# Kernel tuning notes

Measured on AMD Instinct MI355X. Metric: run time of the kernel, lower is better.

## Reference

```python
import jax, jax.numpy as jnp
import numpy as np

# Dimensions
B, T = 4, 512
STOCH = 1024          # flattened stochastic latent dim
D_MODEL = 512
N_LAYER = 4
N_ACT = 16            # discrete action vocab
D_STATE = 16          # SSM state size
K_CONV = 4            # depthwise causal conv width
EXPAND = 2
D_INNER = EXPAND * D_MODEL  # 1024
DT_RANK = D_MODEL // 16     # 32
EPS = 1e-5


def _layer_norm(x, w, b):
    m = jnp.mean(x, axis=-1, keepdims=True)
    v = jnp.mean(jnp.square(x - m), axis=-1, keepdims=True)
    return (x - m) * jax.lax.rsqrt(v + EPS) * w + b


def _mamba_block(x, W_in_l, conv_w_l, conv_b_l, W_xproj_l, W_dt_l, b_dt_l, A_log_l, D_l, W_out_l):
    """Mamba-1 selective-scan block. x: (B,T,d_model) -> (B,T,d_model)."""
    bsz = x.shape[0]
    xz = x @ W_in_l                      # (B,T,2*d_inner)
    xin, z = jnp.split(xz, 2, axis=-1)
    # causal depthwise conv over time
    xc = jnp.transpose(xin, (0, 2, 1))   # (B,d_inner,T)
    xc = jax.lax.conv_general_dilated(
        xc, conv_w_l[:, None, :], (1,), [(K_CONV - 1, 0)],
        dimension_numbers=("NCH", "OIH", "NCH"), feature_group_count=D_INNER)
    xc = xc + conv_b_l[None, :, None]
    xc = jax.nn.silu(jnp.transpose(xc, (0, 2, 1)))   # (B,T,d_inner)
    # input-dependent dt, B, C
    dbc = xc @ W_xproj_l                 # (B,T,dt_rank+2*d_state)
    dt_raw = dbc[..., :DT_RANK]
    Bm = dbc[..., DT_RANK:DT_RANK + D_STATE]
    Cm = dbc[..., DT_RANK + D_STATE:]
    dt = jax.nn.softplus(dt_raw @ W_dt_l + b_dt_l)   # (B,T,d_inner)
    A = -jnp.exp(A_log_l)                # (d_inner,d_state)

    def step(h, inp):
        x_t, dt_t, B_t, C_t = inp        # (B,di),(B,di),(B,ds),(B,ds)
        dA = jnp.exp(dt_t[..., None] * A)                       # (B,di,ds)
        h = dA * h + (dt_t * x_t)[..., None] * B_t[:, None, :]  # (B,di,ds)
        y = jnp.einsum("bds,bs->bd", h, C_t)
        return h, y

    h0 = jnp.zeros((bsz, D_INNER, D_STATE), x.dtype)
    xs = (jnp.swapaxes(xc, 0, 1), jnp.swapaxes(dt, 0, 1),
          jnp.swapaxes(Bm, 0, 1), jnp.swapaxes(Cm, 0, 1))
    _, ys = jax.lax.scan(step, h0, xs)                  # (T,B,d_inner)
    y = jnp.swapaxes(ys, 0, 1) + D_l * xc               # skip connection
    y = y * jax.nn.silu(z)                              # gate
    return y @ W_out_l


def setup_inputs() -> dict:
    key = jax.random.key(0)
    ks = jax.random.split(key, 12)

    def nrm(k, shape, s=0.02):
        return jax.random.normal(k, shape, dtype=jnp.float32) * s

    return {
        "samples": jax.random.normal(ks[0], (B, T, STOCH), dtype=jnp.float32),
        "actions": jax.random.randint(ks[1], (B, T), 0, N_ACT),
        "W_embed": nrm(ks[2], (STOCH, D_MODEL)),
        "b_embed": jnp.zeros((D_MODEL,), jnp.float32),
        "act_embed": nrm(ks[3], (N_ACT, D_MODEL)),
        "ln_w": jnp.ones((N_LAYER, D_MODEL), jnp.float32),
        "ln_b": jnp.zeros((N_LAYER, D_MODEL), jnp.float32),
        "W_in": nrm(ks[4], (N_LAYER, D_MODEL, 2 * D_INNER)),
        "conv_w": nrm(ks[5], (N_LAYER, D_INNER, K_CONV), 0.1),
        "conv_b": jnp.zeros((N_LAYER, D_INNER), jnp.float32),
        "W_xproj": nrm(ks[6], (N_LAYER, D_INNER, DT_RANK + 2 * D_STATE)),
        "W_dt": nrm(ks[7], (N_LAYER, DT_RANK, D_INNER), 0.1),
        "b_dt": jnp.full((N_LAYER, D_INNER), -4.6, jnp.float32),  # softplus ~ 0.01
        "A_log": jnp.log(jnp.broadcast_to(
            jnp.arange(1, D_STATE + 1, dtype=jnp.float32), (N_LAYER, D_INNER, D_STATE))),
        "D_skip": jnp.ones((N_LAYER, D_INNER), jnp.float32),
        "W_out": nrm(ks[8], (N_LAYER, D_INNER, D_MODEL)),
        "normf_w": jnp.ones((D_MODEL,), jnp.float32),
        "normf_b": jnp.zeros((D_MODEL,), jnp.float32),
        "out_ln_w": jnp.ones((D_MODEL,), jnp.float32),
        "out_ln_b": jnp.zeros((D_MODEL,), jnp.float32),
    }


def reference(samples, actions, W_embed, b_embed, act_embed, ln_w, ln_b, W_in,
              conv_w, conv_b, W_xproj, W_dt, b_dt, A_log, D_skip, W_out,
              normf_w, normf_b, out_ln_w, out_ln_b):
    # embed stochastic latent + action token
    x = samples @ W_embed + b_embed + act_embed[actions]   # (B,T,d_model)
    for l in range(N_LAYER):  # structurally distinct layer params; small fixed loop
        x = x + _mamba_block(_layer_norm(x, ln_w[l], ln_b[l]),
                             W_in[l], conv_w[l], conv_b[l], W_xproj[l],
                             W_dt[l], b_dt[l], A_log[l], D_skip[l], W_out[l])
    x = _layer_norm(x, normf_w, normf_b)     # backbone final norm
    x = _layer_norm(x, out_ln_w, out_ln_b)   # adapter output_norm
    return jnp.mean(x, axis=1)               # mean pool over time -> (B,d_model)
```

## Files before the change

### kernel.cpp

```cpp
#include <hip/hip_runtime.h>
#include <hip/hip_bf16.h>
#include <math.h>

#define B_    4
#define T_    512
#define BT    2048
#define STOCH 1024
#define DM    512
#define DI    1024
#define DS    16
#define DTR   32
#define KC    4
#define NL    4
#define EPSV  1e-5f
#define CH    32
#define TC    16
#define SK2   16
#define GKS   4

typedef short bf16x8 __attribute__((ext_vector_type(8)));
typedef float f32x4  __attribute__((ext_vector_type(4)));

__device__ __forceinline__ ushort bfbits(float f) {
    uint u = __float_as_uint(f);
    u += 0x7FFFu + ((u >> 16) & 1u);
    return (ushort)(u >> 16);
}

__global__ __launch_bounds__(256)
void wconvT(const float* __restrict__ W, short* __restrict__ Wt, int K, int N)
{
    const float* Wb = W + (size_t)blockIdx.z * K * N;
    short* Wtb = Wt + (size_t)blockIdx.z * K * N;
    __shared__ float tile[32][33];
    const int tx = threadIdx.x, ty = threadIdx.y;
    const int n0 = blockIdx.x * 32, k0 = blockIdx.y * 32;
    #pragma unroll
    for (int j = 0; j < 4; j++)
        tile[ty + j * 8][tx] = Wb[(size_t)(k0 + ty + j * 8) * N + n0 + tx];
    __syncthreads();
    #pragma unroll
    for (int j = 0; j < 4; j++) {
        const int n = ty + j * 8;
        Wtb[(size_t)(n0 + n) * K + k0 + tx] = (short)bfbits(tile[tx][n]);
    }
}

__global__ __launch_bounds__(256, 4)
void gemm_mfma_sk(const float* __restrict__ A, int lda,
                  const short* __restrict__ Wt, int ldw,
                  float* __restrict__ part, int Ncols, size_t strideZ,
                  int Ksl)
{
    constexpr int BM = 64, BN = 64;
    __shared__ short As[2][BM][40];
    __shared__ short Bs[2][BN][40];
    const int tid = threadIdx.x;
    const int wave = tid >> 6, lane = tid & 63;
    const int lr = lane & 15, lg = lane >> 4;
    const int wm0 = (wave >> 1) * 32, wn0 = (wave & 1) * 32;
    const int bm = blockIdx.y * BM, bn = blockIdx.x * BN;
    const int kbase = blockIdx.z * Ksl;

    f32x4 acc[2][2];
    #pragma unroll
    for (int fi = 0; fi < 2; fi++)
        #pragma unroll
        for (int fj = 0; fj < 2; fj++)
            acc[fi][fj] = (f32x4){0.f, 0.f, 0.f, 0.f};

    float4 ar0, ar1; uint4 br0;
    const int arow0 = tid >> 3, aseg0 = tid & 7;
    const int brow  = tid >> 2, bseg  = tid & 3;

    auto loadT = [&](int k0) {
        ar0 = *reinterpret_cast<const float4*>(A + (size_t)(bm + arow0) * lda + k0 + aseg0 * 4);
        ar1 = *reinterpret_cast<const float4*>(A + (size_t)(bm + arow0 + 32) * lda + k0 + aseg0 * 4);
        br0 = *reinterpret_cast<const uint4*>(Wt + (size_t)(bn + brow) * ldw + k0 + bseg * 8);
    };
    auto storeT = [&](int buf) {
        uint2 p;
        p.x = (uint)bfbits(ar0.x) | ((uint)bfbits(ar0.y) << 16);
        p.y = (uint)bfbits(ar0.z) | ((uint)bfbits(ar0.w) << 16);
        *reinterpret_cast<uint2*>(&As[buf][arow0][aseg0 * 4]) = p;
        p.x = (uint)bfbits(ar1.x) | ((uint)bfbits(ar1.y) << 16);
        p.y = (uint)bfbits(ar1.z) | ((uint)bfbits(ar1.w) << 16);
        *reinterpret_cast<uint2*>(&As[buf][arow0 + 32][aseg0 * 4]) = p;
        *reinterpret_cast<uint4*>(&Bs[buf][brow][bseg * 8]) = br0;
    };

    loadT(kbase);
    storeT(0);
    const int NK = Ksl >> 5;
    for (int kk = 0; kk < NK; kk++) {
        const int cur = kk & 1;
        if (kk + 1 < NK) loadT(kbase + (kk + 1) * 32);
        __syncthreads();
        bf16x8 af[2], bfr[2];
        #pragma unroll
        for (int fi = 0; fi < 2; fi++)
            af[fi] = *reinterpret_cast<const bf16x8*>(&As[cur][wm0 + fi * 16 + lr][lg * 8]);
        #pragma unroll
        for (int fj = 0; fj < 2; fj++)
            bfr[fj] = *reinterpret_cast<const bf16x8*>(&Bs[cur][wn0 + fj * 16 + lr][lg * 8]);
        #pragma unroll
        for (int fi = 0; fi < 2; fi++)
            #pragma unroll
            for (int fj = 0; fj < 2; fj++)
                acc[fi][fj] = __builtin_amdgcn_mfma_f32_16x16x32_bf16(
                    af[fi], bfr[fj], acc[fi][fj], 0, 0, 0);
        if (kk + 1 < NK) storeT(cur ^ 1);
    }

    float* P = part + (size_t)blockIdx.z * strideZ;
    #pragma unroll
    for (int fi = 0; fi < 2; fi++)
        #pragma unroll
        for (int fj = 0; fj < 2; fj++)
            #pragma unroll
            for (int r = 0; r < 4; r++) {
                const int m = bm + wm0 + fi * 16 + lg * 4 + r;
                const int n = bn + wn0 + fj * 16 + lr;
                P[(size_t)m * Ncols + n] = acc[fi][fj][r];
            }
}

__global__ __launch_bounds__(256, 4)
void gemm_mfma_db(const float* __restrict__ A, int lda,
                  const short* __restrict__ Wt, int ldw,
                  float* __restrict__ C, int ldc, int Kd)
{
    constexpr int BM = 64, BN = 64;
    __shared__ short As[2][BM][40];
    __shared__ short Bs[2][BN][40];
    const int tid = threadIdx.x;
    const int wave = tid >> 6, lane = tid & 63;
    const int lr = lane & 15, lg = lane >> 4;
    const int wm0 = (wave >> 1) * 32, wn0 = (wave & 1) * 32;
    const int bm = blockIdx.y * BM, bn = blockIdx.x * BN;

    f32x4 acc[2][2];
    #pragma unroll
    for (int fi = 0; fi < 2; fi++)
        #pragma unroll
        for (int fj = 0; fj < 2; fj++)
            acc[fi][fj] = (f32x4){0.f, 0.f, 0.f, 0.f};

    float4 ar0, ar1; uint4 br0;
    const int arow0 = tid >> 3, aseg0 = tid & 7;
    const int brow  = tid >> 2, bseg  = tid & 3;

    auto loadT = [&](int k0) {
        ar0 = *reinterpret_cast<const float4*>(A + (size_t)(bm + arow0) * lda + k0 + aseg0 * 4);
        ar1 = *reinterpret_cast<const float4*>(A + (size_t)(bm + arow0 + 32) * lda + k0 + aseg0 * 4);
        br0 = *reinterpret_cast<const uint4*>(Wt + (size_t)(bn + brow) * ldw + k0 + bseg * 8);
    };
    auto storeT = [&](int buf) {
        uint2 p;
        p.x = (uint)bfbits(ar0.x) | ((uint)bfbits(ar0.y) << 16);
        p.y = (uint)bfbits(ar0.z) | ((uint)bfbits(ar0.w) << 16);
        *reinterpret_cast<uint2*>(&As[buf][arow0][aseg0 * 4]) = p;
        p.x = (uint)bfbits(ar1.x) | ((uint)bfbits(ar1.y) << 16);
        p.y = (uint)bfbits(ar1.z) | ((uint)bfbits(ar1.w) << 16);
        *reinterpret_cast<uint2*>(&As[buf][arow0 + 32][aseg0 * 4]) = p;
        *reinterpret_cast<uint4*>(&Bs[buf][brow][bseg * 8]) = br0;
    };

    loadT(0);
    storeT(0);
    const int NK = Kd >> 5;
    for (int kk = 0; kk < NK; kk++) {
        const int cur = kk & 1;
        if (kk + 1 < NK) loadT((kk + 1) * 32);
        __syncthreads();
        bf16x8 af[2], bfr[2];
        #pragma unroll
        for (int fi = 0; fi < 2; fi++)
            af[fi] = *reinterpret_cast<const bf16x8*>(&As[cur][wm0 + fi * 16 + lr][lg * 8]);
        #pragma unroll
        for (int fj = 0; fj < 2; fj++)
            bfr[fj] = *reinterpret_cast<const bf16x8*>(&Bs[cur][wn0 + fj * 16 + lr][lg * 8]);
        #pragma unroll
        for (int fi = 0; fi < 2; fi++)
            #pragma unroll
            for (int fj = 0; fj < 2; fj++)
                acc[fi][fj] = __builtin_amdgcn_mfma_f32_16x16x32_bf16(
                    af[fi], bfr[fj], acc[fi][fj], 0, 0, 0);
        if (kk + 1 < NK) storeT(cur ^ 1);
    }

    #pragma unroll
    for (int fi = 0; fi < 2; fi++)
        #pragma unroll
        for (int fj = 0; fj < 2; fj++)
            #pragma unroll
            for (int r = 0; r < 4; r++) {
                const int m = bm + wm0 + fi * 16 + lg * 4 + r;
                const int n = bn + wn0 + fj * 16 + lr;
                C[(size_t)m * ldc + n] = acc[fi][fj][r];
            }
}

__global__ __launch_bounds__(256, 2)
void xprojconv(const float* __restrict__ xz, const float* __restrict__ cw,
               const float* __restrict__ cb, const short* __restrict__ WxT,
               float* __restrict__ xc, float* __restrict__ part)
{
    __shared__ short As[64][40];
    __shared__ short Bs[64][40];
    const int tid = threadIdx.x;
    const int sk = blockIdx.x;
    const int bm = blockIdx.y * 64;
    const int wave = tid >> 6, lane = tid & 63;
    const int lr = lane & 15, lg = lane >> 4;
    const int wm0 = (wave >> 1) * 32, wn0 = (wave & 1) * 32;

    f32x4 acc[2][2];
    #pragma unroll
    for (int fi = 0; fi < 2; fi++)
        #pragma unroll
        for (int fj = 0; fj < 2; fj++)
            acc[fi][fj] = (f32x4){0.f, 0.f, 0.f, 0.f};

    for (int kk = 0; kk < 2; kk++) {
        #pragma unroll
        for (int g = 0; g < 2; g++) {
            const int gi = tid + g * 256;
            const int row = gi >> 3, seg = gi & 7;
            const int bt = bm + row, t = bt & (T_ - 1);
            const int d4 = sk * 64 + kk * 32 + seg * 4;
            const float4 z = {0.f, 0.f, 0.f, 0.f};
            const float4 L0 = *reinterpret_cast<const float4*>(xz + (size_t)bt * 2048 + d4);
            const float4 L1 = (t >= 1) ? *reinterpret_cast<const float4*>(xz + (size_t)(bt - 1) * 2048 + d4) : z;
            const float4 L2 = (t >= 2) ? *reinterpret_cast<const float4*>(xz + (size_t)(bt - 2) * 2048 + d4) : z;
            const float4 L3 = (t >= 3) ? *reinterpret_cast<const float4*>(xz + (size_t)(bt - 3) * 2048 + d4) : z;
            const float4 cbv = *reinterpret_cast<const float4*>(cb + d4);
            float4 o;
            {
                const float4 w = *reinterpret_cast<const float4*>(cw + (size_t)(d4 + 0) * 4);
                o.x = cbv.x + w.w * L0.x + w.z * L1.x + w.y * L2.x + w.x * L3.x;
            }
            {
                const float4 w = *reinterpret_cast<const float4*>(cw + (size_t)(d4 + 1) * 4);
                o.y = cbv.y + w.w * L0.y + w.z * L1.y + w.y * L2.y + w.x * L3.y;
            }
            {
                const float4 w = *reinterpret_cast<const float4*>(cw + (size_t)(d4 + 2) * 4);
                o.z = cbv.z + w.w * L0.z + w.z * L1.z + w.y * L2.z + w.x * L3.z;
            }
            {
                const float4 w = *reinterpret_cast<const float4*>(cw + (size_t)(d4 + 3) * 4);
                o.w = cbv.w + w.w * L0.w + w.z * L1.w + w.y * L2.w + w.x * L3.w;
            }
            o.x *= 1.f / (1.f + __expf(-o.x));
            o.y *= 1.f / (1.f + __expf(-o.y));
            o.z *= 1.f / (1.f + __expf(-o.z));
            o.w *= 1.f / (1.f + __expf(-o.w));
            *reinterpret_cast<float4*>(xc + (size_t)bt * DI + d4) = o;
            uint2 p;
            p.x = (uint)bfbits(o.x) | ((uint)bfbits(o.y) << 16);
            p.y = (uint)bfbits(o.z) | ((uint)bfbits(o.w) << 16);
            *reinterpret_cast<uint2*>(&As[row][seg * 4]) = p;
        }
        {
            const int row = tid >> 2, seg = tid & 3;
            *reinterpret_cast<uint4*>(&Bs[row][seg * 8]) =
                *reinterpret_cast<const uint4*>(WxT + (size_t)row * DI + sk * 64 + kk * 32 + seg * 8);
        }
        __syncthreads();
        bf16x8 af[2], bfr[2];
        #pragma unroll
        for (int fi = 0; fi < 2; fi++)
            af[fi] = *reinterpret_cast<const bf16x8*>(&As[wm0 + fi * 16 + lr][lg * 8]);
        #pragma unroll
        for (int fj = 0; fj < 2; fj++)
            bfr[fj] = *reinterpret_cast<const bf16x8*>(&Bs[wn0 + fj * 16 + lr][lg * 8]);
        #pragma unroll
        for (int fi = 0; fi < 2; fi++)
            #pragma unroll
            for (int fj = 0; fj < 2; fj++)
                acc[fi][fj] = __builtin_amdgcn_mfma_f32_16x16x32_bf16(
                    af[fi], bfr[fj], acc[fi][fj], 0, 0, 0);
        __syncthreads();
    }

    float* P = part + (size_t)sk * (BT * 64);
    #pragma unroll
    for (int fi = 0; fi < 2; fi++)
        #pragma unroll
        for (int fj = 0; fj < 2; fj++)
            #pragma unroll
            for (int r = 0; r < 4; r++) {
                const int m = bm + wm0 + fi * 16 + lg * 4 + r;
                const int n = wn0 + fj * 16 + lr;
                P[(size_t)m * 64 + n] = acc[fi][fj][r];
            }
}

__global__ __launch_bounds__(256)
void dtred(const float* __restrict__ part, const short* __restrict__ WdT,
           const float* __restrict__ b_dt, float* __restrict__ dbc,
           float* __restrict__ dtb)
{
    __shared__ short As[64][40];
    __shared__ short Bs[64][40];
    const int tid = threadIdx.x;
    const int nb = blockIdx.x;
    const int m0 = blockIdx.y * 64, n0 = nb * 64;
    const int wave = tid >> 6, lane = tid & 63;
    const int lr = lane & 15, lg = lane >> 4;
    const int wm0 = (wave >> 1) * 32, wn0 = (wave & 1) * 32;

    #pragma unroll
    for (int g = 0; g < 2; g++) {
        const int gi = tid + g * 256;
        const int row = gi >> 3, seg = gi & 7;
        float4 s = {0.f, 0.f, 0.f, 0.f};
        #pragma unroll
        for (int z = 0; z < SK2; z++) {
            const float4 p = *reinterpret_cast<const float4*>(
                part + (size_t)z * (BT * 64) + (size_t)(m0 + row) * 64 + seg * 4);
            s.x += p.x; s.y += p.y; s.z += p.z; s.w += p.w;
        }
        uint2 pk;
        pk.x = (uint)bfbits(s.x) | ((uint)bfbits(s.y) << 16);
        pk.y = (uint)bfbits(s.z) | ((uint)bfbits(s.w) << 16);
        *reinterpret_cast<uint2*>(&As[row][seg * 4]) = pk;
    }
    {
        const int row = tid >> 2, seg = tid & 3;
        *reinterpret_cast<uint4*>(&Bs[row][seg * 8]) =
            *reinterpret_cast<const uint4*>(WdT + (size_t)(n0 + row) * DTR + seg * 8);
    }
    if (nb == 0) {
        #pragma unroll
        for (int g = 0; g < 2; g++) {
            const int gi = tid + g * 256;
            const int row = gi >> 3, seg = gi & 7;
            float4 s = {0.f, 0.f, 0.f, 0.f};
            #pragma unroll
            for (int z = 0; z < SK2; z++) {
                const float4 p = *reinterpret_cast<const float4*>(
                    part + (size_t)z * (BT * 64) + (size_t)(m0 + row) * 64 + 32 + seg * 4);
                s.x += p.x; s.y += p.y; s.z += p.z; s.w += p.w;
            }
            *reinterpret_cast<float4*>(dbc + (size_t)(m0 + row) * 64 + 32 + seg * 4) = s;
        }
    }
    __syncthreads();

    bf16x8 af[2], bfr[2];
    f32x4 acc[2][2];
    #pragma unroll
    for (int fi = 0; fi < 2; fi++)
        #pragma unroll
        for (int fj = 0; fj < 2; fj++)
            acc[fi][fj] = (f32x4){0.f, 0.f, 0.f, 0.f};
    #pragma unroll
    for (int fi = 0; fi < 2; fi++)
        af[fi] = *reinterpret_cast<const bf16x8*>(&As[wm0 + fi * 16 + lr][lg * 8]);
    #pragma unroll
    for (int fj = 0; fj < 2; fj++)
        bfr[fj] = *reinterpret_cast<const bf16x8*>(&Bs[wn0 + fj * 16 + lr][lg * 8]);
    #pragma unroll
    for (int fi = 0; fi < 2; fi++)
        #pragma unroll
        for (int fj = 0; fj < 2; fj++)
            acc[fi][fj] = __builtin_amdgcn_mfma_f32_16x16x32_bf16(
                af[fi], bfr[fj], acc[fi][fj], 0, 0, 0);
    #pragma unroll
    for (int fi = 0; fi < 2; fi++)
        #pragma unroll
        for (int fj = 0; fj < 2; fj++)
            #pragma unroll
            for (int r = 0; r < 4; r++) {
                const int m = m0 + wm0 + fi * 16 + lg * 4 + r;
                const int n = n0 + wn0 + fj * 16 + lr;
                float v = acc[fi][fj][r] + b_dt[n];
                v = fmaxf(v, 0.f) + log1pf(__expf(-fabsf(v)));
                dtb[(size_t)m * DI + n] = v;
            }
}

__global__ __launch_bounds__(256)
void scan_passA(const float* __restrict__ dt, const float* __restrict__ xc,
                const float* __restrict__ dbc, const float* __restrict__ A_log,
                float* __restrict__ Aprod, float* __restrict__ hloc)
{
    const int blk = blockIdx.x;
    const int dg = blk & 3;
    const int c  = (blk >> 2) & (CH - 1);
    const int b  = blk >> 7;
    const int d  = dg * 256 + threadIdx.x;
    const size_t base = (size_t)b * T_ + c * TC;

    __shared__ float Bsh[TC][DS];
    {
        const int t = threadIdx.x >> 4, s = threadIdx.x & 15;
        Bsh[t][s] = dbc[(base + t) * 64 + 32 + s];
    }
    __syncthreads();

    float Aval[DS], h[DS], ap[DS];
    #pragma unroll
    for (int s = 0; s < DS; s++) {
        Aval[s] = -__expf(A_log[(size_t)d * DS + s]);
        h[s] = 0.f; ap[s] = 1.f;
    }

    #pragma unroll 4
    for (int t = 0; t < TC; t++) {
        const size_t r = base + t;
        const float dtv = dt[r * DI + d];
        const float xv  = xc[r * DI + d];
        const float u = dtv * xv;
        #pragma unroll
        for (int s = 0; s < DS; s++) {
            const float a = __expf(dtv * Aval[s]);
            h[s] = a * h[s] + u * Bsh[t][s];
            ap[s] *= a;
        }
    }
    const size_t o0 = ((size_t)(b * CH + c) * DS) * DI + d;
    #pragma unroll
    for (int s = 0; s < DS; s++) {
        Aprod[o0 + (size_t)s * DI] = ap[s];
        hloc[o0 + (size_t)s * DI]  = h[s];
    }
}

__global__ __launch_bounds__(256)
void scan_passB(const float* __restrict__ Aprod, float* __restrict__ hloc)
{
    const int idx = blockIdx.x * 256 + threadIdx.x;
    const int d = idx & (DI - 1);
    const int s = (idx >> 10) & (DS - 1);
    const int b = idx >> 14;
    float h = 0.f;
    for (int c = 0; c < CH; c++) {
        const size_t o = ((size_t)(b * CH + c) * DS + s) * DI + d;
        const float a  = Aprod[o];
        const float hl = hloc[o];
        hloc[o] = h;
        h = a * h + hl;
    }
}

__global__ __launch_bounds__(256)
void scan_passC(const float* __restrict__ dt, const float* __restrict__ xc,
                const float* __restrict__ dbc, const float* __restrict__ xz,
                const float* __restrict__ A_log, const float* __restrict__ Dskip,
                const float* __restrict__ h0buf, float* __restrict__ y)
{
    const int blk = blockIdx.x;
    const int dg = blk & 3;
    const int c  = (blk >> 2) & (CH - 1);
    const int b  = blk >> 7;
    const int d  = dg * 256 + threadIdx.x;
    const size_t base = (size_t)b * T_ + c * TC;

    __shared__ float Bsh[TC][DS];
    __shared__ float Csh[TC][DS];
    for (int i = threadIdx.x; i < TC * 32; i += 256) {
        const int t = i >> 5, sc = i & 31;
        const float v = dbc[(base + t) * 64 + 32 + sc];
        if (sc < 16) Bsh[t][sc] = v; else Csh[t][sc - 16] = v;
    }
    __syncthreads();

    float Aval[DS], h[DS];
    const size_t o0 = ((size_t)(b * CH + c) * DS) * DI + d;
    #pragma unroll
    for (int s = 0; s < DS; s++) {
        Aval[s] = -__expf(A_log[(size_t)d * DS + s]);
        h[s] = h0buf[o0 + (size_t)s * DI];
    }
    const float Dv = Dskip[d];

    #pragma unroll 2
    for (int t = 0; t < TC; t++) {
        const size_t r = base + t;
        const float dtv = dt[r * DI + d];
        const float xv  = xc[r * DI + d];
        const float u = dtv * xv;
        float yacc = 0.f;
        #pragma unroll
        for (int s = 0; s < DS; s++) {
            const float a = __expf(dtv * Aval[s]);
            h[s] = a * h[s] + u * Bsh[t][s];
            yacc += h[s] * Csh[t][s];
        }
        const float zv = xz[r * 2048 + 1024 + d];
        const float sg = 1.f / (1.f + __expf(-zv));
        y[r * DI + d] = (yacc + Dv * xv) * (zv * sg);
    }
}

template<int MODE>
__global__ __launch_bounds__(256)
void red_ln(const float* __restrict__ part, float* __restrict__ x,
            float* __restrict__ hout,
            const float* __restrict__ e1, const float* __restrict__ e2,
            const int* __restrict__ act,
            const float* __restrict__ w1, const float* __restrict__ b1,
            const float* __restrict__ w2, const float* __restrict__ b2)
{
    const int row = blockIdx.x, tid = threadIdx.x;
    const size_t ro = (size_t)row * DM;
    __shared__ float sm[4], sm2[4];
    float v[2];
    float s = 0.f, ss = 0.f;
    #pragma unroll
    for (int g = 0; g < 2; g++) {
        const int c = tid + g * 256;
        float t = 0.f;
        #pragma unroll
        for (int z = 0; z < GKS; z++) t += part[(size_t)z * (BT * DM) + ro + c];
        if (MODE == 0) t += e1[c] + e2[(size_t)act[row] * DM + c];
        else           t += x[ro + c];
        if (MODE != 2) x[ro + c] = t;
        v[g] = t; s += t; ss += t * t;
    }
    #pragma unroll
    for (int m = 32; m >= 1; m >>= 1) { s += __shfl_xor(s, m, 64); ss += __shfl_xor(ss, m, 64); }
    if ((tid & 63) == 0) { sm[tid >> 6] = s; sm2[tid >> 6] = ss; }
    __syncthreads();
    s  = sm[0] + sm[1] + sm[2] + sm[3];
    ss = sm2[0] + sm2[1] + sm2[2] + sm2[3];
    float mean = s * (1.f / DM);
    float var = fmaxf(ss * (1.f / DM) - mean * mean, 0.f);
    float rstd = rsqrtf(var + EPSV);
    if (MODE < 2) {
        #pragma unroll
        for (int g = 0; g < 2; g++) {
            const int c = tid + g * 256;
            hout[ro + c] = (v[g] - mean) * rstd * w1[c] + b1[c];
        }
    } else {
        float u[2]; float s2 = 0.f, ss2 = 0.f;
        #pragma unroll
        for (int g = 0; g < 2; g++) {
            const int c = tid + g * 256;
            u[g] = (v[g] - mean) * rstd * w1[c] + b1[c];
            s2 += u[g]; ss2 += u[g] * u[g];
        }
        #pragma unroll
        for (int m = 32; m >= 1; m >>= 1) { s2 += __shfl_xor(s2, m, 64); ss2 += __shfl_xor(ss2, m, 64); }
        __syncthreads();
        if ((tid & 63) == 0) { sm[tid >> 6] = s2; sm2[tid >> 6] = ss2; }
        __syncthreads();
        s2  = sm[0] + sm[1] + sm[2] + sm[3];
        ss2 = sm2[0] + sm2[1] + sm2[2] + sm2[3];
        float mean2 = s2 * (1.f / DM);
        float var2 = fmaxf(ss2 * (1.f / DM) - mean2 * mean2, 0.f);
        float rstd2 = rsqrtf(var2 + EPSV);
        #pragma unroll
        for (int g = 0; g < 2; g++) {
            const int c = tid + g * 256;
            hout[ro + c] = (u[g] - mean2) * rstd2 * w2[c] + b2[c];
        }
    }
}

__global__ __launch_bounds__(256)
void mean_kernel(const float* __restrict__ x, float* __restrict__ out)
{
    const int idx = blockIdx.x * 256 + threadIdx.x;
    const int b = idx / DM;
    const int dcol = idx % DM;
    float ssum = 0.f;
    for (int t = 0; t < T_; t++) ssum += x[((size_t)b * T_ + t) * DM + dcol];
    out[idx] = ssum * (1.f / T_);
}

extern "C" void kernel_launch(void* const* d_in, const int* in_sizes, int n_in,
                              void* d_out, int out_size, void* d_ws, size_t ws_size,
                              hipStream_t stream)
{
    const float* samples  = (const float*)d_in[0];
    const int*   actions  = (const int*)  d_in[1];
    const float* W_embed  = (const float*)d_in[2];
    const float* b_embed  = (const float*)d_in[3];
    const float* act_emb  = (const float*)d_in[4];
    const float* ln_w     = (const float*)d_in[5];
    const float* ln_b     = (const float*)d_in[6];
    const float* W_in     = (const float*)d_in[7];
    const float* conv_w   = (const float*)d_in[8];
    const float* conv_b   = (const float*)d_in[9];
    const float* W_xproj  = (const float*)d_in[10];
    const float* W_dt     = (const float*)d_in[11];
    const float* b_dt     = (const float*)d_in[12];
    const float* A_log    = (const float*)d_in[13];
    const float* D_skip   = (const float*)d_in[14];
    const float* W_out    = (const float*)d_in[15];
    const float* normf_w  = (const float*)d_in[16];
    const float* normf_b  = (const float*)d_in[17];
    const float* out_ln_w = (const float*)d_in[18];
    const float* out_ln_b = (const float*)d_in[19];

    float* ws  = (float*)d_ws;
    float* x    = ws;
    float* h    = x    + (size_t)BT * DM;
    float* xz   = h    + (size_t)BT * DM;
    float* xc   = xz   + (size_t)BT * 2048;
    float* dbc  = xc   + (size_t)BT * DI;
    float* dtb  = dbc  + (size_t)BT * 64;
    float* yg   = dtb  + (size_t)BT * DI;
    float* Apr  = yg   + (size_t)BT * DI;
    float* hlo  = Apr  + (size_t)B_ * CH * DI * DS;
    float* xpart = Apr;
    float* gpart = Apr;
    float* wb   = hlo  + (size_t)B_ * CH * DI * DS;
    short* WtE  = (short*)wb;
    short* WtI  = WtE + (size_t)DM * STOCH;
    short* WtO  = WtI + (size_t)4 * 2048 * DM;
    short* WxT  = WtO + (size_t)4 * DM * DI;
    short* WdT  = WxT + (size_t)4 * 64 * DI;

    const int MN = BT * DM;

    wconvT<<<dim3(DM / 32, STOCH / 32, 1), dim3(32, 8), 0, stream>>>(W_embed, WtE, STOCH, DM);
    wconvT<<<dim3(2048 / 32, DM / 32, 4), dim3(32, 8), 0, stream>>>(W_in, WtI, DM, 2048);
    wconvT<<<dim3(DM / 32, DI / 32, 4), dim3(32, 8), 0, stream>>>(W_out, WtO, DI, DM);
    wconvT<<<dim3(64 / 32, DI / 32, 4), dim3(32, 8), 0, stream>>>(W_xproj, WxT, DI, 64);
    wconvT<<<dim3(DI / 32, 1, 4), dim3(32, 8), 0, stream>>>(W_dt, WdT, DTR, DI);

    gemm_mfma_sk<<<dim3(DM / 64, BT / 64, GKS), 256, 0, stream>>>(
        samples, STOCH, WtE, STOCH, gpart, DM, (size_t)MN, STOCH / GKS);
    red_ln<0><<<BT, 256, 0, stream>>>(gpart, x, h, b_embed, act_emb, actions,
                                      ln_w, ln_b, nullptr, nullptr);

    for (int l = 0; l < NL; l++) {
        gemm_mfma_db<<<dim3(2048 / 64, BT / 64), 256, 0, stream>>>(
            h, DM, WtI + (size_t)l * 2048 * DM, DM, xz, 2048, DM);
        xprojconv<<<dim3(SK2, BT / 64), 256, 0, stream>>>(
            xz, conv_w + (size_t)l * DI * KC, conv_b + (size_t)l * DI,
            WxT + (size_t)l * 64 * DI, xc, xpart);
        dtred<<<dim3(16, BT / 64), 256, 0, stream>>>(
            xpart, WdT + (size_t)l * DI * DTR, b_dt + (size_t)l * DI, dbc, dtb);
        scan_passA<<<B_ * CH * (DI / 256), 256, 0, stream>>>(
            dtb, xc, dbc, A_log + (size_t)l * DI * DS, Apr, hlo);
        scan_passB<<<(B_ * DS * DI) / 256, 256, 0, stream>>>(Apr, hlo);
        scan_passC<<<B_ * CH * (DI / 256), 256, 0, stream>>>(
            dtb, xc, dbc, xz, A_log + (size_t)l * DI * DS, D_skip + (size_t)l * DI,
            hlo, yg);
        gemm_mfma_sk<<<dim3(DM / 64, BT / 64, GKS), 256, 0, stream>>>(
            yg, DI, WtO + (size_t)l * DM * DI, DI, gpart, DM, (size_t)MN, DI / GKS);
        if (l < NL - 1)
            red_ln<1><<<BT, 256, 0, stream>>>(gpart, x, h, nullptr, nullptr, nullptr,
                                              ln_w + (size_t)(l + 1) * DM,
                                              ln_b + (size_t)(l + 1) * DM,
                                              nullptr, nullptr);
        else
            red_ln<2><<<BT, 256, 0, stream>>>(gpart, x, yg, nullptr, nullptr, nullptr,
                                              normf_w, normf_b, out_ln_w, out_ln_b);
    }

    mean_kernel<<<(B_ * DM) / 256, 256, 0, stream>>>(yg, (float*)d_out);
}
```

Before: 467.0 us.

## Atomic-accumulate out-projection split-K into residual and merge weight conversion launches

The out-projection split-K GEMM now adds its partial sums straight into the residual stream x with float atomics, instead of writing four partial buffers that red_ln later reads and sums. red_ln in the layer modes then only reads x. Separately, the five weight transpose-and-convert launches are merged into one kernel that picks its source matrix from the block index. This removes partial-buffer traffic and launch overhead, but makes the summation order nondeterministic and adds atomic contention.

```diff
diff --git a/kernel.cpp b/kernel.cpp
--- a/kernel.cpp
+++ b/kernel.cpp
@@ -27,22 +27,42 @@
     return (ushort)(u >> 16);
 }
 
+#define TE_ 512
+#define TI_ 4096
+#define TO_ 2048
+#define TX_ 256
+#define TD_ 128
 __global__ __launch_bounds__(256)
-void wconvT(const float* __restrict__ W, short* __restrict__ Wt, int K, int N)
-{
-    const float* Wb = W + (size_t)blockIdx.z * K * N;
-    short* Wtb = Wt + (size_t)blockIdx.z * K * N;
+void wconvT_all(const float* __restrict__ We, short* __restrict__ WtE,
+                const float* __restrict__ Wi, short* __restrict__ WtI,
+                const float* __restrict__ Wo, short* __restrict__ WtO,
+                const float* __restrict__ Wx, short* __restrict__ WxT,
+                const float* __restrict__ Wd, short* __restrict__ WdT)
+{
+    int t = blockIdx.x;
+    const float* W; short* Wt; int K, N;
+    if (t < TE_)                         { W = We; Wt = WtE; K = STOCH; N = DM; }
+    else if ((t -= TE_) < TI_)           { W = Wi; Wt = WtI; K = DM;    N = 2048; }
+    else if ((t -= TI_) < TO_)           { W = Wo; Wt = WtO; K = DI;    N = DM; }
+    else if ((t -= TO_) < TX_)           { W = Wx; Wt = WxT; K = DI;    N = 64; }
+    else       { t -= TX_;                 W = Wd; Wt = WdT; K = DTR;   N = DI; }
+    const int ntx = N >> 5, per = (N >> 5) * (K >> 5);
+    const int batch = t / per;  t %= per;
+    const int bx = t % ntx, by = t / ntx;
+    W  += (size_t)batch * K * N;
+    Wt += (size_t)batch * K * N;
+
     __shared__ float tile[32][33];
     const int tx = threadIdx.x, ty = threadIdx.y;
-    const int n0 = blockIdx.x * 32, k0 = blockIdx.y * 32;
+    const int n0 = bx * 32, k0 = by * 32;
     #pragma unroll
     for (int j = 0; j < 4; j++)
-        tile[ty + j * 8][tx] = Wb[(size_t)(k0 + ty + j * 8) * N + n0 + tx];
+        tile[ty + j * 8][tx] = W[(size_t)(k0 + ty + j * 8) * N + n0 + tx];
     __syncthreads();
     #pragma unroll
     for (int j = 0; j < 4; j++) {
         const int n = ty + j * 8;
-        Wtb[(size_t)(n0 + n) * K + k0 + tx] = (short)bfbits(tile[tx][n]);
+        Wt[(size_t)(n0 + n) * K + k0 + tx] = (short)bfbits(tile[tx][n]);
     }
 }
 
@@ -126,9 +146,9 @@
 }
 
 __global__ __launch_bounds__(256, 4)
-void gemm_mfma_db(const float* __restrict__ A, int lda,
+void gemm_mfma_at(const float* __restrict__ A, int lda,
                   const short* __restrict__ Wt, int ldw,
-                  float* __restrict__ C, int ldc, int Kd)
+                  float* __restrict__ C, int Ncols, int Ksl)
 {
     constexpr int BM = 64, BN = 64;
     __shared__ short As[2][BM][40];
@@ -138,6 +158,7 @@
     const int lr = lane & 15, lg = lane >> 4;
     const int wm0 = (wave >> 1) * 32, wn0 = (wave & 1) * 32;
     const int bm = blockIdx.y * BM, bn = blockIdx.x * BN;
+    const int kbase = blockIdx.z * Ksl;
 
     f32x4 acc[2][2];
     #pragma unroll
@@ -166,6 +187,82 @@
         *reinterpret_cast<uint4*>(&Bs[buf][brow][bseg * 8]) = br0;
     };
 
+    loadT(kbase);
+    storeT(0);
+    const int NK = Ksl >> 5;
+    for (int kk = 0; kk < NK; kk++) {
+        const int cur = kk & 1;
+        if (kk + 1 < NK) loadT(kbase + (kk + 1) * 32);
+        __syncthreads();
+        bf16x8 af[2], bfr[2];
+        #pragma unroll
+        for (int fi = 0; fi < 2; fi++)
+            af[fi] = *reinterpret_cast<const bf16x8*>(&As[cur][wm0 + fi * 16 + lr][lg * 8]);
+        #pragma unroll
+        for (int fj = 0; fj < 2; fj++)
+            bfr[fj] = *reinterpret_cast<const bf16x8*>(&Bs[cur][wn0 + fj * 16 + lr][lg * 8]);
+        #pragma unroll
+        for (int fi = 0; fi < 2; fi++)
+            #pragma unroll
+            for (int fj = 0; fj < 2; fj++)
+                acc[fi][fj] = __builtin_amdgcn_mfma_f32_16x16x32_bf16(
+                    af[fi], bfr[fj], acc[fi][fj], 0, 0, 0);
+        if (kk + 1 < NK) storeT(cur ^ 1);
+    }
+
+    #pragma unroll
+    for (int fi = 0; fi < 2; fi++)
+        #pragma unroll
+        for (int fj = 0; fj < 2; fj++)
+            #pragma unroll
+            for (int r = 0; r < 4; r++) {
+                const int m = bm + wm0 + fi * 16 + lg * 4 + r;
+                const int n = bn + wn0 + fj * 16 + lr;
+                unsafeAtomicAdd(&C[(size_t)m * Ncols + n], acc[fi][fj][r]);
+            }
+}
+
+__global__ __launch_bounds__(256, 4)
+void gemm_mfma_db(const float* __restrict__ A, int lda,
+                  const short* __restrict__ Wt, int ldw,
+                  float* __restrict__ C, int ldc, int Kd)
+{
+    constexpr int BM = 64, BN = 64;
+    __shared__ short As[2][BM][40];
+    __shared__ short Bs[2][BN][40];
+    const int tid = threadIdx.x;
+    const int wave = tid >> 6, lane = tid & 63;
+    const int lr = lane & 15, lg = lane >> 4;
+    const int wm0 = (wave >> 1) * 32, wn0 = (wave & 1) * 32;
+    const int bm = blockIdx.y * BM, bn = blockIdx.x * BN;
+
+    f32x4 acc[2][2];
+    #pragma unroll
+    for (int fi = 0; fi < 2; fi++)
+        #pragma unroll
+        for (int fj = 0; fj < 2; fj++)
+            acc[fi][fj] = (f32x4){0.f, 0.f, 0.f, 0.f};
+
+    float4 ar0, ar1; uint4 br0;
+    const int arow0 = tid >> 3, aseg0 = tid & 7;
+    const int brow  = tid >> 2, bseg  = tid & 3;
+
+    auto loadT = [&](int k0) {
+        ar0 = *reinterpret_cast<const float4*>(A + (size_t)(bm + arow0) * lda + k0 + aseg0 * 4);
+        ar1 = *reinterpret_cast<const float4*>(A + (size_t)(bm + arow0 + 32) * lda + k0 + aseg0 * 4);
+        br0 = *reinterpret_cast<const uint4*>(Wt + (size_t)(bn + brow) * ldw + k0 + bseg * 8);
+    };
+    auto storeT = [&](int buf) {
+        uint2 p;
+        p.x = (uint)bfbits(ar0.x) | ((uint)bfbits(ar0.y) << 16);
+        p.y = (uint)bfbits(ar0.z) | ((uint)bfbits(ar0.w) << 16);
+        *reinterpret_cast<uint2*>(&As[buf][arow0][aseg0 * 4]) = p;
+        p.x = (uint)bfbits(ar1.x) | ((uint)bfbits(ar1.y) << 16);
+        p.y = (uint)bfbits(ar1.z) | ((uint)bfbits(ar1.w) << 16);
+        *reinterpret_cast<uint2*>(&As[buf][arow0 + 32][aseg0 * 4]) = p;
+        *reinterpret_cast<uint4*>(&Bs[buf][brow][bseg * 8]) = br0;
+    };
+
     loadT(0);
     storeT(0);
     const int NK = Kd >> 5;
@@ -513,12 +610,16 @@
     #pragma unroll
     for (int g = 0; g < 2; g++) {
         const int c = tid + g * 256;
-        float t = 0.f;
-        #pragma unroll
-        for (int z = 0; z < GKS; z++) t += part[(size_t)z * (BT * DM) + ro + c];
-        if (MODE == 0) t += e1[c] + e2[(size_t)act[row] * DM + c];
-        else           t += x[ro + c];
-        if (MODE != 2) x[ro + c] = t;
+        float t;
+        if (MODE == 0) {
+            t = 0.f;
+            #pragma unroll
+            for (int z = 0; z < GKS; z++) t += part[(size_t)z * (BT * DM) + ro + c];
+            t += e1[c] + e2[(size_t)act[row] * DM + c];
+            x[ro + c] = t;
+        } else {
+            t = x[ro + c];
+        }
         v[g] = t; s += t; ss += t * t;
     }
     #pragma unroll
@@ -619,11 +720,8 @@
 
     const int MN = BT * DM;
 
-    wconvT<<<dim3(DM / 32, STOCH / 32, 1), dim3(32, 8), 0, stream>>>(W_embed, WtE, STOCH, DM);
-    wconvT<<<dim3(2048 / 32, DM / 32, 4), dim3(32, 8), 0, stream>>>(W_in, WtI, DM, 2048);
-    wconvT<<<dim3(DM / 32, DI / 32, 4), dim3(32, 8), 0, stream>>>(W_out, WtO, DI, DM);
-    wconvT<<<dim3(64 / 32, DI / 32, 4), dim3(32, 8), 0, stream>>>(W_xproj, WxT, DI, 64);
-    wconvT<<<dim3(DI / 32, 1, 4), dim3(32, 8), 0, stream>>>(W_dt, WdT, DTR, DI);
+    wconvT_all<<<TE_ + TI_ + TO_ + TX_ + TD_, dim3(32, 8), 0, stream>>>(
+        W_embed, WtE, W_in, WtI, W_out, WtO, W_xproj, WxT, W_dt, WdT);
 
     gemm_mfma_sk<<<dim3(DM / 64, BT / 64, GKS), 256, 0, stream>>>(
         samples, STOCH, WtE, STOCH, gpart, DM, (size_t)MN, STOCH / GKS);
@@ -644,15 +742,15 @@
         scan_passC<<<B_ * CH * (DI / 256), 256, 0, stream>>>(
             dtb, xc, dbc, xz, A_log + (size_t)l * DI * DS, D_skip + (size_t)l * DI,
             hlo, yg);
-        gemm_mfma_sk<<<dim3(DM / 64, BT / 64, GKS), 256, 0, stream>>>(
-            yg, DI, WtO + (size_t)l * DM * DI, DI, gpart, DM, (size_t)MN, DI / GKS);
+        gemm_mfma_at<<<dim3(DM / 64, BT / 64, GKS), 256, 0, stream>>>(
+            yg, DI, WtO + (size_t)l * DM * DI, DI, x, DM, DI / GKS);
         if (l < NL - 1)
-            red_ln<1><<<BT, 256, 0, stream>>>(gpart, x, h, nullptr, nullptr, nullptr,
+            red_ln<1><<<BT, 256, 0, stream>>>(nullptr, x, h, nullptr, nullptr, nullptr,
                                               ln_w + (size_t)(l + 1) * DM,
                                               ln_b + (size_t)(l + 1) * DM,
                                               nullptr, nullptr);
         else
-            red_ln<2><<<BT, 256, 0, stream>>>(gpart, x, yg, nullptr, nullptr, nullptr,
+            red_ln<2><<<BT, 256, 0, stream>>>(nullptr, x, yg, nullptr, nullptr, nullptr,
                                               normf_w, normf_b, out_ln_w, out_ln_b);
     }
 
```

After: 480.7 us. 2.9% more time.

## Fold chunk-carry scan into passC and merge weight conversion launches

Applied to the files above, without the earlier changes.

Removes the separate scan_passB kernel: each passC block now recomputes its incoming state by sequentially combining all prior chunks' Aprod/hloc summaries. This drops one launch and a read-modify-write pass over the chunk summaries per layer, but it adds redundant work that grows with chunk index, so late chunks read up to 31×16 values per thread. Separately, the five weight transpose/convert launches are merged into one flat-grid kernel that dispatches on block index.

```diff
diff --git a/kernel.cpp b/kernel.cpp
--- a/kernel.cpp
+++ b/kernel.cpp
@@ -27,22 +27,42 @@
     return (ushort)(u >> 16);
 }
 
+#define TE_ 512
+#define TI_ 4096
+#define TO_ 2048
+#define TX_ 256
+#define TD_ 128
 __global__ __launch_bounds__(256)
-void wconvT(const float* __restrict__ W, short* __restrict__ Wt, int K, int N)
-{
-    const float* Wb = W + (size_t)blockIdx.z * K * N;
-    short* Wtb = Wt + (size_t)blockIdx.z * K * N;
+void wconvT_all(const float* __restrict__ We, short* __restrict__ WtE,
+                const float* __restrict__ Wi, short* __restrict__ WtI,
+                const float* __restrict__ Wo, short* __restrict__ WtO,
+                const float* __restrict__ Wx, short* __restrict__ WxT,
+                const float* __restrict__ Wd, short* __restrict__ WdT)
+{
+    int t = blockIdx.x;
+    const float* W; short* Wt; int K, N;
+    if (t < TE_)                         { W = We; Wt = WtE; K = STOCH; N = DM; }
+    else if ((t -= TE_) < TI_)           { W = Wi; Wt = WtI; K = DM;    N = 2048; }
+    else if ((t -= TI_) < TO_)           { W = Wo; Wt = WtO; K = DI;    N = DM; }
+    else if ((t -= TO_) < TX_)           { W = Wx; Wt = WxT; K = DI;    N = 64; }
+    else       { t -= TX_;                 W = Wd; Wt = WdT; K = DTR;   N = DI; }
+    const int ntx = N >> 5, per = (N >> 5) * (K >> 5);
+    const int batch = t / per;  t %= per;
+    const int bx = t % ntx, by = t / ntx;
+    W  += (size_t)batch * K * N;
+    Wt += (size_t)batch * K * N;
+
     __shared__ float tile[32][33];
     const int tx = threadIdx.x, ty = threadIdx.y;
-    const int n0 = blockIdx.x * 32, k0 = blockIdx.y * 32;
+    const int n0 = bx * 32, k0 = by * 32;
     #pragma unroll
     for (int j = 0; j < 4; j++)
-        tile[ty + j * 8][tx] = Wb[(size_t)(k0 + ty + j * 8) * N + n0 + tx];
+        tile[ty + j * 8][tx] = W[(size_t)(k0 + ty + j * 8) * N + n0 + tx];
     __syncthreads();
     #pragma unroll
     for (int j = 0; j < 4; j++) {
         const int n = ty + j * 8;
-        Wtb[(size_t)(n0 + n) * K + k0 + tx] = (short)bfbits(tile[tx][n]);
+        Wt[(size_t)(n0 + n) * K + k0 + tx] = (short)bfbits(tile[tx][n]);
     }
 }
 
@@ -430,27 +450,11 @@
 }
 
 __global__ __launch_bounds__(256)
-void scan_passB(const float* __restrict__ Aprod, float* __restrict__ hloc)
-{
-    const int idx = blockIdx.x * 256 + threadIdx.x;
-    const int d = idx & (DI - 1);
-    const int s = (idx >> 10) & (DS - 1);
-    const int b = idx >> 14;
-    float h = 0.f;
-    for (int c = 0; c < CH; c++) {
-        const size_t o = ((size_t)(b * CH + c) * DS + s) * DI + d;
-        const float a  = Aprod[o];
-        const float hl = hloc[o];
-        hloc[o] = h;
-        h = a * h + hl;
-    }
-}
-
-__global__ __launch_bounds__(256)
 void scan_passC(const float* __restrict__ dt, const float* __restrict__ xc,
                 const float* __restrict__ dbc, const float* __restrict__ xz,
                 const float* __restrict__ A_log, const float* __restrict__ Dskip,
-                const float* __restrict__ h0buf, float* __restrict__ y)
+                const float* __restrict__ Aprod, const float* __restrict__ hloc,
+                float* __restrict__ y)
 {
     const int blk = blockIdx.x;
     const int dg = blk & 3;
@@ -469,11 +473,19 @@
     __syncthreads();
 
     float Aval[DS], h[DS];
-    const size_t o0 = ((size_t)(b * CH + c) * DS) * DI + d;
+    const size_t o0 = ((size_t)b * CH * DS) * DI + d;
     #pragma unroll
     for (int s = 0; s < DS; s++) {
         Aval[s] = -__expf(A_log[(size_t)d * DS + s]);
-        h[s] = h0buf[o0 + (size_t)s * DI];
+        h[s] = 0.f;
+    }
+    for (int cc = 0; cc < c; cc++) {
+        const size_t oc = o0 + (size_t)cc * DS * DI;
+        #pragma unroll
+        for (int s = 0; s < DS; s++) {
+            const size_t o = oc + (size_t)s * DI;
+            h[s] = Aprod[o] * h[s] + hloc[o];
+        }
     }
     const float Dv = Dskip[d];
 
@@ -619,11 +631,8 @@
 
     const int MN = BT * DM;
 
-    wconvT<<<dim3(DM / 32, STOCH / 32, 1), dim3(32, 8), 0, stream>>>(W_embed, WtE, STOCH, DM);
-    wconvT<<<dim3(2048 / 32, DM / 32, 4), dim3(32, 8), 0, stream>>>(W_in, WtI, DM, 2048);
-    wconvT<<<dim3(DM / 32, DI / 32, 4), dim3(32, 8), 0, stream>>>(W_out, WtO, DI, DM);
-    wconvT<<<dim3(64 / 32, DI / 32, 4), dim3(32, 8), 0, stream>>>(W_xproj, WxT, DI, 64);
-    wconvT<<<dim3(DI / 32, 1, 4), dim3(32, 8), 0, stream>>>(W_dt, WdT, DTR, DI);
+    wconvT_all<<<TE_ + TI_ + TO_ + TX_ + TD_, dim3(32, 8), 0, stream>>>(
+        W_embed, WtE, W_in, WtI, W_out, WtO, W_xproj, WxT, W_dt, WdT);
 
     gemm_mfma_sk<<<dim3(DM / 64, BT / 64, GKS), 256, 0, stream>>>(
         samples, STOCH, WtE, STOCH, gpart, DM, (size_t)MN, STOCH / GKS);
@@ -640,10 +649,9 @@
             xpart, WdT + (size_t)l * DI * DTR, b_dt + (size_t)l * DI, dbc, dtb);
         scan_passA<<<B_ * CH * (DI / 256), 256, 0, stream>>>(
             dtb, xc, dbc, A_log + (size_t)l * DI * DS, Apr, hlo);
-        scan_passB<<<(B_ * DS * DI) / 256, 256, 0, stream>>>(Apr, hlo);
         scan_passC<<<B_ * CH * (DI / 256), 256, 0, stream>>>(
             dtb, xc, dbc, xz, A_log + (size_t)l * DI * DS, D_skip + (size_t)l * DI,
-            hlo, yg);
+            Apr, hlo, yg);
         gemm_mfma_sk<<<dim3(DM / 64, BT / 64, GKS), 256, 0, stream>>>(
             yg, DI, WtO + (size_t)l * DM * DI, DI, gpart, DM, (size_t)MN, DI / GKS);
         if (l < NL - 1)
```

New measurement: 508.4 us. 8.9% more time.
